# Performance work log

Hardware: AMD Instinct MI355X
Metric: run time of the kernel (lower is better)

## Reference

```python
import jax, jax.numpy as jnp
import numpy as np

B, D, N, H = 4, 512, 1536, 8
DIM = D // H  # per-head dim = 64


def _conv1x1(x, w, b):
    # Conv1d(kernel_size=1): x [B, C, N], w [O, C], b [O]
    return jnp.einsum('oc,bcn->bon', w, x) + b[None, :, None]


def setup_inputs() -> dict:
    key = jax.random.key(0)
    ks = jax.random.split(key, 13)
    s = 0.02
    return {
        'query': jax.random.normal(ks[0], (B, D, N), jnp.float32),
        'key': jax.random.normal(ks[1], (B, D, N), jnp.float32),
        'value': jax.random.normal(ks[2], (B, D, N), jnp.float32),
        'dist': jax.random.uniform(ks[3], (B, N, N), jnp.float32),
        'mask': jax.random.bernoulli(ks[4], 0.9, (N, N)),  # bool [N, M]
        'Wq': jax.random.normal(ks[5], (D, D), jnp.float32) * s,
        'bq': jnp.zeros((D,), jnp.float32),
        'Wk': jax.random.normal(ks[6], (D, D), jnp.float32) * s,
        'bk': jnp.zeros((D,), jnp.float32),
        'Wv': jax.random.normal(ks[7], (D, D), jnp.float32) * s,
        'bv': jnp.zeros((D,), jnp.float32),
        'Wm': jax.random.normal(ks[8], (D, D), jnp.float32) * s,
        'bm': jnp.zeros((D,), jnp.float32),
    }


def reference(query, key, value, dist, mask, Wq, bq, Wk, bk, Wv, bv, Wm, bm):
    # dist is accepted but unused, exactly as in the original forward.
    q = _conv1x1(query, Wq, bq).reshape(B, DIM, H, N)
    k = _conv1x1(key, Wk, bk).reshape(B, DIM, H, N)
    v = _conv1x1(value, Wv, bv).reshape(B, DIM, H, N)
    scores = jnp.einsum('bdhn,bdhm->bhnm', q, k) / jnp.sqrt(jnp.float32(DIM))
    # custom additive mask: (detached global min - 20) on masked-out positions
    pen = (jax.lax.stop_gradient(scores.min()) - 20.0) * (~mask).astype(scores.dtype)
    scores = scores + pen[None, None]  # broadcast over [B, H]
    prob = jax.nn.softmax(scores, axis=-1)
    x = jnp.einsum('bhnm,bdhm->bdhn', prob, v).reshape(B, D, N)
    out = _conv1x1(x, Wm, bm)
    return out, scores.mean(axis=1)
```

## Files before the change

### kernel.cpp

```cpp
#include <hip/hip_runtime.h>
#include <hip/hip_bf16.h>

typedef __hip_bfloat16 bf16;
typedef __attribute__((ext_vector_type(8))) short s16x8;
typedef __attribute__((ext_vector_type(4))) float f32x4;
typedef unsigned char uchar;

#define B_   4
#define D_   512
#define N_   1536
#define H_   8
#define DIM_ 64
#define NN_  (N_*N_)
#define BIGNEG (-30000.0f)

#define MFMA(a,b,c) __builtin_amdgcn_mfma_f32_16x16x32_bf16((a),(b),(c),0,0,0)

__device__ __forceinline__ short b16(float x){ bf16 h = __float2bfloat16(x); return *reinterpret_cast<short*>(&h); }

__device__ __forceinline__ s16x8 w8(const float* p){
  float4 u = *(const float4*)p, v = *(const float4*)(p+4);
  s16x8 r;
  r[0]=b16(u.x); r[1]=b16(u.y); r[2]=b16(u.z); r[3]=b16(u.w);
  r[4]=b16(v.x); r[5]=b16(v.y); r[6]=b16(v.z); r[7]=b16(v.w);
  return r;
}

__device__ unsigned detect_w4(const uchar* __restrict__ mraw, int* sh, int t){
  if (t == 0){ sh[0] = 0; sh[1] = 0; }
  __syncthreads();
  int a = 0, bb = 0;
  for (int i = t; i < 4096; i += 256){
    uchar v = mraw[i];
    if (v > 1) a = 1;
    else if (v && (i & 3)) bb = 1;
  }
  if (a)  atomicOr(&sh[0], 1);
  if (bb) atomicOr(&sh[1], 1);
  __syncthreads();
  return sh[0] ? 1u : (sh[1] ? 0u : 1u);
}

__global__ void detect_k(const uchar* __restrict__ mraw, unsigned* __restrict__ flags){
  __shared__ int sh[2];
  unsigned w4 = detect_w4(mraw, sh, threadIdx.x);
  if (threadIdx.x == 0) flags[0] = w4;
}

__global__ __launch_bounds__(256) void cvtW_k(const float* __restrict__ W0, const float* __restrict__ W1,
                                              const float* __restrict__ W2, const float* __restrict__ W3,
                                              bf16* __restrict__ dst){
  const float* src = (blockIdx.y==0)?W0:(blockIdx.y==1)?W1:(blockIdx.y==2)?W2:W3;
  bf16* d = dst + (size_t)blockIdx.y*(D_*D_);
  int i = (blockIdx.x*256 + threadIdx.x)*4;
  float4 v = *(const float4*)(src + i);
  __align__(8) short tmp[4] = {b16(v.x), b16(v.y), b16(v.z), b16(v.w)};
  *(int2*)((short*)d + i) = *(const int2*)tmp;
}

__device__ __forceinline__ void load_mt(uchar (*mt)[64], const void* mraw, unsigned w4,
                                        int n0, int m0, int t){
  int row = t >> 2, c = (t & 3) * 16;
  if (!w4){
    *(int4*)&mt[row][c] = *(const int4*)((const uchar*)mraw + (size_t)(n0 + row)*N_ + m0 + c);
  } else {
    const unsigned* mp = (const unsigned*)mraw + (size_t)(n0 + row)*N_ + m0 + c;
    uchar tmp[16];
    #pragma unroll
    for (int j = 0; j < 16; ++j) tmp[j] = mp[j] ? 1 : 0;
    *(int4*)&mt[row][c] = *(const int4*)tmp;
  }
}

__device__ __forceinline__ int mask_at(const void* mraw, unsigned w4, int n, int m){
  if (w4) return ((const unsigned*)mraw)[(size_t)n*N_ + m] != 0;
  return ((const uchar*)mraw)[(size_t)n*N_ + m] != 0;
}

template<int WBF>
__global__ __launch_bounds__(256) void convQKf_k(const float* __restrict__ X, const float* __restrict__ Wf,
                                                 const bf16* __restrict__ Wb,
                                                 const float* __restrict__ bias, bf16* __restrict__ dst,
                                                 float scale){
  int b = blockIdx.z, ot = blockIdx.y, nt = blockIdx.x;
  int t = threadIdx.x, w = t >> 6, L = t & 63, g = L >> 4, q = L & 15;
  __shared__ short Xs[64][72];
  __shared__ short tile[64][72];
  f32x4 acc[4] = {};
  float4 pf[4];
  #pragma unroll
  for (int it = 0; it < 4; ++it){
    int i = it*256 + t, cc = i >> 4, nq = (i & 15)*4;
    pf[it] = *(const float4*)(X + ((size_t)b*D_ + cc)*N_ + nt*64 + nq);
  }
  for (int cs = 0; cs < 8; ++cs){
    __syncthreads();
    #pragma unroll
    for (int it = 0; it < 4; ++it){
      int i = it*256 + t, cc = i >> 4, nq = (i & 15)*4;
      Xs[nq+0][cc] = b16(pf[it].x); Xs[nq+1][cc] = b16(pf[it].y);
      Xs[nq+2][cc] = b16(pf[it].z); Xs[nq+3][cc] = b16(pf[it].w);
    }
    if (cs < 7){
      #pragma unroll
      for (int it = 0; it < 4; ++it){
        int i = it*256 + t, cc = i >> 4, nq = (i & 15)*4;
        pf[it] = *(const float4*)(X + ((size_t)b*D_ + (cs+1)*64 + cc)*N_ + nt*64 + nq);
      }
    }
    __syncthreads();
    #pragma unroll
    for (int kk = 0; kk < 64; kk += 32){
      s16x8 a = *(const s16x8*)&Xs[w*16 + q][kk + 8*g];
      #pragma unroll
      for (int f = 0; f < 4; ++f){
        s16x8 bb;
        if (WBF) bb = *(const s16x8*)(Wb + (size_t)(ot*64 + f*16 + q)*D_ + cs*64 + kk + 8*g);
        else     bb = w8(Wf + (size_t)(ot*64 + f*16 + q)*D_ + cs*64 + kk + 8*g);
        acc[f] = MFMA(a, bb, acc[f]);
      }
    }
  }
  #pragma unroll
  for (int f = 0; f < 4; ++f){
    float bv = bias[ot*64 + f*16 + q];
    #pragma unroll
    for (int r = 0; r < 4; ++r)
      tile[w*16 + 4*g + r][f*16 + q] = b16((acc[f][r] + bv)*scale);
  }
  __syncthreads();
  #pragma unroll
  for (int it = 0; it < 2; ++it){
    int s = t + 256*it, row = s >> 3, h = s & 7;
    short tmp[8];
    #pragma unroll
    for (int j = 0; j < 8; ++j) tmp[j] = tile[row][h + 8*j];
    *(int4*)((short*)dst + ((size_t)(b*8+h)*N_ + nt*64 + row)*DIM_ + ot*8) = *(const int4*)tmp;
  }
}

template<int WBF>
__global__ __launch_bounds__(256) void convVf_k(const float* __restrict__ X, const float* __restrict__ Wf,
                                                const bf16* __restrict__ Wb,
                                                const float* __restrict__ bias, bf16* __restrict__ dst){
  int b = blockIdx.z, ot = blockIdx.y, nt = blockIdx.x;
  int t = threadIdx.x, w = t >> 6, L = t & 63, g = L >> 4, q = L & 15;
  __shared__ short Xs[64][72];
  __shared__ short tile[64][72];
  f32x4 acc[4] = {};
  float4 pf[4];
  #pragma unroll
  for (int it = 0; it < 4; ++it){
    int i = it*256 + t, cc = i >> 4, nq = (i & 15)*4;
    pf[it] = *(const float4*)(X + ((size_t)b*D_ + cc)*N_ + nt*64 + nq);
  }
  for (int cs = 0; cs < 8; ++cs){
    __syncthreads();
    #pragma unroll
    for (int it = 0; it < 4; ++it){
      int i = it*256 + t, cc = i >> 4, nq = (i & 15)*4;
      Xs[nq+0][cc] = b16(pf[it].x); Xs[nq+1][cc] = b16(pf[it].y);
      Xs[nq+2][cc] = b16(pf[it].z); Xs[nq+3][cc] = b16(pf[it].w);
    }
    if (cs < 7){
      #pragma unroll
      for (int it = 0; it < 4; ++it){
        int i = it*256 + t, cc = i >> 4, nq = (i & 15)*4;
        pf[it] = *(const float4*)(X + ((size_t)b*D_ + (cs+1)*64 + cc)*N_ + nt*64 + nq);
      }
    }
    __syncthreads();
    #pragma unroll
    for (int kk = 0; kk < 64; kk += 32){
      s16x8 a = *(const s16x8*)&Xs[w*16 + q][kk + 8*g];
      #pragma unroll
      for (int f = 0; f < 4; ++f){
        s16x8 bb;
        if (WBF) bb = *(const s16x8*)(Wb + (size_t)(ot*64 + f*16 + q)*D_ + cs*64 + kk + 8*g);
        else     bb = w8(Wf + (size_t)(ot*64 + f*16 + q)*D_ + cs*64 + kk + 8*g);
        acc[f] = MFMA(a, bb, acc[f]);
      }
    }
  }
  #pragma unroll
  for (int f = 0; f < 4; ++f){
    float bv = bias[ot*64 + f*16 + q];
    #pragma unroll
    for (int r = 0; r < 4; ++r)
      tile[w*16 + 4*g + r][f*16 + q] = b16(acc[f][r] + bv);
  }
  __syncthreads();
  int col = t & 63, seg = t >> 6;
  int h = col & 7, d = ot*8 + (col >> 3);
  short tmp[16];
  #pragma unroll
  for (int j = 0; j < 16; ++j) tmp[j] = tile[seg*16 + j][col];
  short* p = (short*)dst + ((size_t)(b*8+h)*DIM_ + d)*N_ + nt*64 + seg*16;
  *(int4*)p       = *(const int4*)&tmp[0];
  *(int4*)(p + 8) = *(const int4*)&tmp[8];
}

__global__ __launch_bounds__(256) void passA_k(const bf16* __restrict__ QH, const bf16* __restrict__ KH,
                                               float* __restrict__ out2f, float* __restrict__ bmin){
  int b = blockIdx.z, ntb = blockIdx.y, mtb = blockIdx.x;
  int t = threadIdx.x, w = t >> 6, L = t & 63, g = L >> 4, q = L & 15;
  __shared__ short Ks[2][64][72];
  int r0 = t >> 3, s0 = (t & 7)*8, r1 = (t + 256) >> 3;
  f32x4 mean[4] = {};
  float vmin = 3.4e38f;
  {
    const bf16* kb = KH + ((size_t)(b*H_)*N_ + mtb*64)*DIM_;
    *(int4*)&Ks[0][r0][s0] = *(const int4*)(kb + (size_t)r0*DIM_ + s0);
    *(int4*)&Ks[0][r1][s0] = *(const int4*)(kb + (size_t)r1*DIM_ + s0);
  }
  const bf16* qrow0 = QH + ((size_t)(b*H_)*N_ + ntb*64 + w*16 + q)*DIM_;
  s16x8 qa0 = *(const s16x8*)(qrow0 + 8*g);
  s16x8 qa1 = *(const s16x8*)(qrow0 + 32 + 8*g);
  int4 kn0, kn1; s16x8 qn0, qn1;
  {
    const bf16* kb = KH + ((size_t)(b*H_ + 1)*N_ + mtb*64)*DIM_;
    kn0 = *(const int4*)(kb + (size_t)r0*DIM_ + s0);
    kn1 = *(const int4*)(kb + (size_t)r1*DIM_ + s0);
    const bf16* qrow = QH + ((size_t)(b*H_ + 1)*N_ + ntb*64 + w*16 + q)*DIM_;
    qn0 = *(const s16x8*)(qrow + 8*g);
    qn1 = *(const s16x8*)(qrow + 32 + 8*g);
  }
  __syncthreads();
  for (int h = 0; h < H_; ++h){
    f32x4 acc[4] = {};
    #pragma unroll
    for (int f = 0; f < 4; ++f){
      acc[f] = MFMA(qa0, *(const s16x8*)&Ks[h&1][f*16 + q][8*g], acc[f]);
      acc[f] = MFMA(qa1, *(const s16x8*)&Ks[h&1][f*16 + q][32 + 8*g], acc[f]);
    }
    if (h < H_-1){
      *(int4*)&Ks[(h+1)&1][r0][s0] = kn0;
      *(int4*)&Ks[(h+1)&1][r1][s0] = kn1;
      qa0 = qn0; qa1 = qn1;
      if (h < H_-2){
        const bf16* kb = KH + ((size_t)(b*H_ + h+2)*N_ + mtb*64)*DIM_;
        kn0 = *(const int4*)(kb + (size_t)r0*DIM_ + s0);
        kn1 = *(const int4*)(kb + (size_t)r1*DIM_ + s0);
        const bf16* qrow = QH + ((size_t)(b*H_ + h+2)*N_ + ntb*64 + w*16 + q)*DIM_;
        qn0 = *(const s16x8*)(qrow + 8*g);
        qn1 = *(const s16x8*)(qrow + 32 + 8*g);
      }
    }
    #pragma unroll
    for (int f = 0; f < 4; ++f){
      #pragma unroll
      for (int r = 0; r < 4; ++r) vmin = fminf(vmin, acc[f][r]);
      mean[f] += acc[f];
    }
    __syncthreads();
  }
  #pragma unroll
  for (int off = 32; off; off >>= 1) vmin = fminf(vmin, __shfl_xor(vmin, off));
  __shared__ float wmin[4];
  if (L == 0) wmin[w] = vmin;
  __syncthreads();
  if (t == 0)
    bmin[((size_t)b*24 + ntb)*24 + mtb] = fminf(fminf(wmin[0],wmin[1]), fminf(wmin[2],wmin[3]));
  #pragma unroll
  for (int f = 0; f < 4; ++f)
    #pragma unroll
    for (int r = 0; r < 4; ++r)
      out2f[(size_t)b*NN_ + (size_t)(ntb*64 + w*16 + 4*g + r)*N_ + mtb*64 + f*16 + q]
        = mean[f][r] * 0.125f;
}

__global__ void minred_k(const float* __restrict__ bmin, float* __restrict__ penp){
  int t = threadIdx.x;
  float m = 3.4e38f;
  for (int i = t; i < 2304; i += 256) m = fminf(m, bmin[i]);
  #pragma unroll
  for (int off = 32; off; off >>= 1) m = fminf(m, __shfl_xor(m, off));
  __shared__ float wm[4];
  if ((t & 63) == 0) wm[t >> 6] = m;
  __syncthreads();
  if (t == 0) penp[0] = fminf(fminf(wm[0],wm[1]), fminf(wm[2],wm[3])) - 20.0f;
}

__global__ __launch_bounds__(256) void passCf_k(const void* __restrict__ mraw,
                                                const unsigned* __restrict__ flags,
                                                const float* __restrict__ penp,
                                                float* __restrict__ out2f){
  int i = blockIdx.x*256 + threadIdx.x;
  if (i >= NN_) return;
  int keep = flags[0] ? (((const unsigned*)mraw)[i] != 0) : (((const uchar*)mraw)[i] != 0);
  if (keep) return;
  float pen = penp[0];
  #pragma unroll
  for (int b = 0; b < B_; ++b) out2f[(size_t)b*NN_ + i] += pen;
}

__global__ __launch_bounds__(256) void passB_k(const bf16* __restrict__ QH, const bf16* __restrict__ KH,
                                               const bf16* __restrict__ VT, const void* __restrict__ mraw,
                                               bf16* __restrict__ xT){
  int b = blockIdx.z, h = blockIdx.y, ntb = blockIdx.x;
  int t = threadIdx.x, w = t >> 6, L = t & 63, g = L >> 4, q = L & 15;
  __shared__ short Ks[64][72], Vs[64][72];
  __shared__ uchar mt[64][64];
  __shared__ short P[4][16][72];
  __shared__ int dsh[2];
  unsigned w4 = detect_w4((const uchar*)mraw, dsh, t);
  size_t bh = (size_t)(b*H_ + h);
  const bf16* kbase = KH + bh*N_*DIM_;
  const bf16* vbase = VT + bh*(size_t)DIM_*N_;
  const bf16* qrow = QH + (bh*N_ + ntb*64 + w*16 + q)*DIM_;
  s16x8 qa0 = *(const s16x8*)(qrow + 8*g);
  s16x8 qa1 = *(const s16x8*)(qrow + 32 + 8*g);
  int r0 = t >> 3, s0 = (t & 7)*8, r1 = (t + 256) >> 3;
  int mrow = t >> 2, mc = (t & 3)*16;
  int4 kreg0, kreg1, vreg0, vreg1, mreg4[4];
  float lacc[4] = {0.f,0.f,0.f,0.f};
  f32x4 O[4] = {};
  {
    kreg0 = *(const int4*)(kbase + (size_t)r0*DIM_ + s0);
    kreg1 = *(const int4*)(kbase + (size_t)r1*DIM_ + s0);
    vreg0 = *(const int4*)(vbase + (size_t)r0*N_ + s0);
    vreg1 = *(const int4*)(vbase + (size_t)r1*N_ + s0);
    if (!w4) mreg4[0] = *(const int4*)((const uchar*)mraw + (size_t)(ntb*64 + mrow)*N_ + mc);
    else {
      const int4* mp = (const int4*)((const unsigned*)mraw + (size_t)(ntb*64 + mrow)*N_ + mc);
      #pragma unroll
      for (int j = 0; j < 4; ++j) mreg4[j] = mp[j];
    }
  }
  for (int mtb = 0; mtb < 24; ++mtb){
    __syncthreads();
    *(int4*)&Ks[r0][s0] = kreg0;
    *(int4*)&Ks[r1][s0] = kreg1;
    *(int4*)&Vs[r0][s0] = vreg0;
    *(int4*)&Vs[r1][s0] = vreg1;
    if (!w4) *(int4*)&mt[mrow][mc] = mreg4[0];
    else {
      uchar tmp[16];
      #pragma unroll
      for (int j = 0; j < 16; ++j) tmp[j] = ((const unsigned*)mreg4)[j] ? 1 : 0;
      *(int4*)&mt[mrow][mc] = *(const int4*)tmp;
    }
    if (mtb < 23){
      int m0 = (mtb+1)*64;
      kreg0 = *(const int4*)(kbase + (size_t)(m0 + r0)*DIM_ + s0);
      kreg1 = *(const int4*)(kbase + (size_t)(m0 + r1)*DIM_ + s0);
      vreg0 = *(const int4*)(vbase + (size_t)r0*N_ + m0 + s0);
      vreg1 = *(const int4*)(vbase + (size_t)r1*N_ + m0 + s0);
      if (!w4) mreg4[0] = *(const int4*)((const uchar*)mraw + (size_t)(ntb*64 + mrow)*N_ + m0 + mc);
      else {
        const int4* mp = (const int4*)((const unsigned*)mraw + (size_t)(ntb*64 + mrow)*N_ + m0 + mc);
        #pragma unroll
        for (int j = 0; j < 4; ++j) mreg4[j] = mp[j];
      }
    }
    __syncthreads();
    f32x4 acc[4] = {};
    #pragma unroll
    for (int f = 0; f < 4; ++f){
      acc[f] = MFMA(qa0, *(const s16x8*)&Ks[f*16 + q][8*g], acc[f]);
      acc[f] = MFMA(qa1, *(const s16x8*)&Ks[f*16 + q][32 + 8*g], acc[f]);
    }
    float pv[4][4];
    #pragma unroll
    for (int f = 0; f < 4; ++f)
      #pragma unroll
      for (int r = 0; r < 4; ++r)
        pv[f][r] = mt[w*16 + 4*g + r][f*16 + q] ? __expf(acc[f][r]) : 0.0f;
    #pragma unroll
    for (int r = 0; r < 4; ++r)
      lacc[r] += (pv[0][r] + pv[1][r]) + (pv[2][r] + pv[3][r]);
    #pragma unroll
    for (int f = 0; f < 4; ++f)
      #pragma unroll
      for (int r = 0; r < 4; ++r)
        P[w][4*g + r][f*16 + q] = b16(pv[f][r]);
    #pragma unroll
    for (int f2 = 0; f2 < 4; ++f2){
      O[f2] = MFMA(*(const s16x8*)&P[w][q][8*g],      *(const s16x8*)&Vs[f2*16 + q][8*g],      O[f2]);
      O[f2] = MFMA(*(const s16x8*)&P[w][q][32 + 8*g], *(const s16x8*)&Vs[f2*16 + q][32 + 8*g], O[f2]);
    }
  }
  #pragma unroll
  for (int r = 0; r < 4; ++r){
    #pragma unroll
    for (int off = 1; off < 16; off <<= 1) lacc[r] += __shfl_xor(lacc[r], off);
  }
  float inv[4];
  #pragma unroll
  for (int r = 0; r < 4; ++r) inv[r] = 1.0f / lacc[r];
  #pragma unroll
  for (int f2 = 0; f2 < 4; ++f2)
    #pragma unroll
    for (int r = 0; r < 4; ++r){
      int n = ntb*64 + w*16 + 4*g + r, d = f2*16 + q;
      ((short*)xT)[((size_t)b*N_ + n)*D_ + d*8 + h] = b16(O[f2][r]*inv[r]);
    }
}

template<int WBF>
__global__ __launch_bounds__(256) void gemm2_k(const float* __restrict__ Wmf, const bf16* __restrict__ Wmb,
                                               const float* __restrict__ bm,
                                               const bf16* __restrict__ xT, float* __restrict__ out0f){
  int b = blockIdx.z, ot = blockIdx.y, nt = blockIdx.x;
  int t = threadIdx.x, w = t >> 6, L = t & 63, g = L >> 4, q = L & 15;
  f32x4 acc[4] = {};
  for (int kk = 0; kk < D_; kk += 32){
    s16x8 a;
    if (WBF) a = *(const s16x8*)(Wmb + (size_t)(ot*64 + w*16 + q)*D_ + kk + 8*g);
    else     a = w8(Wmf + (size_t)(ot*64 + w*16 + q)*D_ + kk + 8*g);
    #pragma unroll
    for (int f = 0; f < 4; ++f){
      s16x8 bb = *(const s16x8*)(xT + ((size_t)b*N_ + nt*64 + f*16 + q)*D_ + kk + 8*g);
      acc[f] = MFMA(a, bb, acc[f]);
    }
  }
  #pragma unroll
  for (int f = 0; f < 4; ++f)
    #pragma unroll
    for (int r = 0; r < 4; ++r){
      int o = ot*64 + w*16 + 4*g + r;
      out0f[((size_t)b*D_ + o)*N_ + nt*64 + f*16 + q] = acc[f][r] + bm[o];
    }
}

__global__ __launch_bounds__(256) void t64_k(const float* __restrict__ X, bf16* __restrict__ XT){
  int b = blockIdx.z, ct = blockIdx.y, nt = blockIdx.x, t = threadIdx.x;
  __shared__ bf16 T[64][72];
  #pragma unroll
  for (int it = 0; it < 4; ++it){
    int idx = t + 256*it, cc = idx >> 4, s = idx & 15;
    float4 v = *(const float4*)(X + ((size_t)b*D_ + ct*64 + cc)*N_ + nt*64 + s*4);
    T[cc][s*4+0] = __float2bfloat16(v.x);
    T[cc][s*4+1] = __float2bfloat16(v.y);
    T[cc][s*4+2] = __float2bfloat16(v.z);
    T[cc][s*4+3] = __float2bfloat16(v.w);
  }
  __syncthreads();
  #pragma unroll
  for (int it = 0; it < 2; ++it){
    int idx = t + 256*it, nn = idx >> 3, s = idx & 7;
    short tmp[8];
    #pragma unroll
    for (int j = 0; j < 8; ++j) tmp[j] = *(short*)&T[s*8 + j][nn];
    *(int4*)((short*)XT + ((size_t)b*N_ + nt*64 + nn)*D_ + ct*64 + s*8) = *(const int4*)tmp;
  }
}

__global__ __launch_bounds__(256) void convQK_k(const bf16* __restrict__ XT, const float* __restrict__ W,
                                                const float* __restrict__ bias, bf16* __restrict__ dst,
                                                float scale){
  int b = blockIdx.z, ot = blockIdx.y, nt = blockIdx.x;
  int t = threadIdx.x, w = t >> 6, L = t & 63, g = L >> 4, q = L & 15;
  const bf16* Arow = XT + ((size_t)b*N_ + nt*64 + w*16 + q)*D_;
  f32x4 acc[4] = {};
  for (int kk = 0; kk < D_; kk += 32){
    s16x8 a = *(const s16x8*)(Arow + kk + 8*g);
    #pragma unroll
    for (int f = 0; f < 4; ++f){
      s16x8 bb = w8(W + (size_t)(ot*64 + f*16 + q)*D_ + kk + 8*g);
      acc[f] = MFMA(a, bb, acc[f]);
    }
  }
  __shared__ short tile[64][72];
  #pragma unroll
  for (int f = 0; f < 4; ++f){
    float bv = bias[ot*64 + f*16 + q];
    #pragma unroll
    for (int r = 0; r < 4; ++r)
      tile[w*16 + 4*g + r][f*16 + q] = b16((acc[f][r] + bv)*scale);
  }
  __syncthreads();
  #pragma unroll
  for (int it = 0; it < 2; ++it){
    int s = t + 256*it, row = s >> 3, h = s & 7;
    short tmp[8];
    #pragma unroll
    for (int j = 0; j < 8; ++j) tmp[j] = tile[row][h + 8*j];
    *(int4*)((short*)dst + ((size_t)(b*8+h)*N_ + nt*64 + row)*DIM_ + ot*8) = *(const int4*)tmp;
  }
}

__global__ __launch_bounds__(256) void convV_k(const bf16* __restrict__ XT, const float* __restrict__ W,
                                               const float* __restrict__ bias, bf16* __restrict__ dst){
  int b = blockIdx.z, ot = blockIdx.y, nt = blockIdx.x;
  int t = threadIdx.x, w = t >> 6, L = t & 63, g = L >> 4, q = L & 15;
  const bf16* Arow = XT + ((size_t)b*N_ + nt*64 + w*16 + q)*D_;
  f32x4 acc[4] = {};
  for (int kk = 0; kk < D_; kk += 32){
    s16x8 a = *(const s16x8*)(Arow + kk + 8*g);
    #pragma unroll
    for (int f = 0; f < 4; ++f){
      s16x8 bb = w8(W + (size_t)(ot*64 + f*16 + q)*D_ + kk + 8*g);
      acc[f] = MFMA(a, bb, acc[f]);
    }
  }
  __shared__ short tile[64][72];
  #pragma unroll
  for (int f = 0; f < 4; ++f){
    float bv = bias[ot*64 + f*16 + q];
    #pragma unroll
    for (int r = 0; r < 4; ++r)
      tile[w*16 + 4*g + r][f*16 + q] = b16(acc[f][r] + bv);
  }
  __syncthreads();
  int col = t & 63, seg = t >> 6;
  int h = col & 7, d = ot*8 + (col >> 3);
  short tmp[16];
  #pragma unroll
  for (int j = 0; j < 16; ++j) tmp[j] = tile[seg*16 + j][col];
  short* p = (short*)dst + ((size_t)(b*8+h)*DIM_ + d)*N_ + nt*64 + seg*16;
  *(int4*)p       = *(const int4*)&tmp[0];
  *(int4*)(p + 8) = *(const int4*)&tmp[8];
}

__global__ __launch_bounds__(256) void min_k(const bf16* __restrict__ QH, const bf16* __restrict__ KH,
                                             float* __restrict__ bmin){
  int b = blockIdx.z, ntb = blockIdx.y, mtb = blockIdx.x;
  int t = threadIdx.x, w = t >> 6, L = t & 63, g = L >> 4, q = L & 15;
  float vmin = 3.4e38f;
  for (int h = 0; h < H_; ++h){
    size_t bh = (size_t)(b*H_ + h);
    const bf16* qrow = QH + (bh*N_ + ntb*64 + w*16 + q)*DIM_;
    const bf16* krow = KH + (bh*N_ + mtb*64 + q)*DIM_;
    f32x4 acc[4] = {};
    #pragma unroll
    for (int kk = 0; kk < 64; kk += 32){
      s16x8 a = *(const s16x8*)(qrow + kk + 8*g);
      #pragma unroll
      for (int f = 0; f < 4; ++f){
        s16x8 bb = *(const s16x8*)(krow + (size_t)f*16*DIM_ + kk + 8*g);
        acc[f] = MFMA(a, bb, acc[f]);
      }
    }
    #pragma unroll
    for (int f = 0; f < 4; ++f)
      #pragma unroll
      for (int r = 0; r < 4; ++r) vmin = fminf(vmin, acc[f][r]);
  }
  #pragma unroll
  for (int off = 32; off; off >>= 1) vmin = fminf(vmin, __shfl_xor(vmin, off));
  __shared__ float wmin[4];
  if (L == 0) wmin[w] = vmin;
  __syncthreads();
  if (t == 0)
    bmin[((size_t)b*24 + ntb)*24 + mtb] = fminf(fminf(wmin[0],wmin[1]), fminf(wmin[2],wmin[3]));
}

__global__ __launch_bounds__(256) void meanLow_k(const bf16* __restrict__ QH, const bf16* __restrict__ KH,
                                                 const void* __restrict__ mraw, const float* __restrict__ penp,
                                                 float* __restrict__ out2f){
  int mtb = blockIdx.x, rt = blockIdx.y;
  if (rt == 48 && mtb == 0) return;
  __shared__ uchar mt[64][64];
  __shared__ int dsh[2];
  int t = threadIdx.x, w = t >> 6, L = t & 63, g = L >> 4, q = L & 15;
  unsigned w4 = detect_w4((const uchar*)mraw, dsh, t);
  int gr = rt*64, b = gr / N_, n0 = gr % N_;
  load_mt(mt, mraw, w4, n0, mtb*64, t);
  __syncthreads();
  float pen = penp[0];
  f32x4 mean[4] = {};
  for (int h = 0; h < H_; ++h){
    size_t bh = (size_t)(b*H_ + h);
    const bf16* qrow = QH + (bh*N_ + n0 + w*16 + q)*DIM_;
    const bf16* krow = KH + (bh*N_ + mtb*64 + q)*DIM_;
    f32x4 acc[4] = {};
    #pragma unroll
    for (int kk = 0; kk < 64; kk += 32){
      s16x8 a = *(const s16x8*)(qrow + kk + 8*g);
      #pragma unroll
      for (int f = 0; f < 4; ++f){
        s16x8 bb = *(const s16x8*)(krow + (size_t)f*16*DIM_ + kk + 8*g);
        acc[f] = MFMA(a, bb, acc[f]);
      }
    }
    #pragma unroll
    for (int f = 0; f < 4; ++f) mean[f] += acc[f];
  }
  #pragma unroll
  for (int f = 0; f < 4; ++f)
    #pragma unroll
    for (int r = 0; r < 4; ++r){
      float v = mean[f][r]*0.125f;
      if (!mt[w*16 + 4*g + r][f*16 + q]) v += pen;
      out2f[(size_t)b*NN_ + (size_t)(n0 + w*16 + 4*g + r)*N_ + mtb*64 + f*16 + q] = v;
    }
}

__device__ void build_head(const float* __restrict__ X, const float* __restrict__ W,
                           const float* __restrict__ bias, int b, int n0, int h,
                           short (*dst)[72], short (*Xs)[72], int t){
  int w = t >> 6, L = t & 63, g = L >> 4, q = L & 15;
  f32x4 acc[4] = {};
  for (int cs = 0; cs < 8; ++cs){
    __syncthreads();
    #pragma unroll
    for (int it = 0; it < 4; ++it){
      int i = it*256 + t, cc = i >> 4, nq = (i & 15)*4;
      float4 v = *(const float4*)(X + ((size_t)b*D_ + cs*64 + cc)*N_ + n0 + nq);
      Xs[nq+0][cc] = b16(v.x); Xs[nq+1][cc] = b16(v.y);
      Xs[nq+2][cc] = b16(v.z); Xs[nq+3][cc] = b16(v.w);
    }
    __syncthreads();
    #pragma unroll
    for (int kk = 0; kk < 64; kk += 32){
      s16x8 a = w8(W + (size_t)((w*16 + q)*8 + h)*D_ + cs*64 + kk + 8*g);
      #pragma unroll
      for (int f = 0; f < 4; ++f){
        s16x8 bb = *(const s16x8*)&Xs[f*16 + q][kk + 8*g];
        acc[f] = MFMA(a, bb, acc[f]);
      }
    }
  }
  __syncthreads();
  #pragma unroll
  for (int f = 0; f < 4; ++f)
    #pragma unroll
    for (int r = 0; r < 4; ++r){
      int d = w*16 + 4*g + r, n = f*16 + q;
      dst[n][d] = b16(acc[f][r] + bias[d*8 + h]);
    }
  __syncthreads();
}

__global__ __launch_bounds__(256) void meanHigh_k(const float* __restrict__ Xq, const float* __restrict__ Wq,
                                                  const float* __restrict__ bq,
                                                  const float* __restrict__ Xk, const float* __restrict__ Wk,
                                                  const float* __restrict__ bk,
                                                  const void* __restrict__ mraw, const float* __restrict__ penp,
                                                  float* __restrict__ out2f){
  __shared__ short qt[64][72], kt[64][72], Xs[64][72];
  __shared__ int dsh[2];
  int t = threadIdx.x, w = t >> 6, L = t & 63, g = L >> 4, q = L & 15;
  unsigned w4 = detect_w4((const uchar*)mraw, dsh, t);
  int rt = 64 + blockIdx.y, gr = rt*64, b = gr / N_, n0 = gr % N_;
  float pen = penp[0];
  f32x4 mean[6][4] = {};
  for (int h = 0; h < H_; ++h){
    build_head(Xq, Wq, bq, b, n0, h, qt, Xs, t);
    for (int mi = 0; mi < 6; ++mi){
      int m0 = (blockIdx.x*6 + mi)*64;
      build_head(Xk, Wk, bk, b, m0, h, kt, Xs, t);
      f32x4 acc[4] = {};
      #pragma unroll
      for (int kk = 0; kk < 64; kk += 32){
        s16x8 a = *(const s16x8*)&qt[w*16 + q][kk + 8*g];
        #pragma unroll
        for (int f = 0; f < 4; ++f){
          s16x8 bb = *(const s16x8*)&kt[f*16 + q][kk + 8*g];
          acc[f] = MFMA(a, bb, acc[f]);
        }
      }
      #pragma unroll
      for (int f = 0; f < 4; ++f) mean[mi][f] += acc[f]*0.125f;
    }
  }
  for (int mi = 0; mi < 6; ++mi){
    int m0 = (blockIdx.x*6 + mi)*64;
    #pragma unroll
    for (int f = 0; f < 4; ++f)
      #pragma unroll
      for (int r = 0; r < 4; ++r){
        int n = n0 + w*16 + 4*g + r, m = m0 + f*16 + q;
        float v = mean[mi][f][r]*0.125f;
        if (!mask_at(mraw, w4, n, m)) v += pen;
        out2f[(size_t)b*NN_ + (size_t)n*N_ + m] = v;
      }
  }
}

__global__ __launch_bounds__(256) void meanFinal_k(const float* __restrict__ Xq, const float* __restrict__ Wq,
                                                   const float* __restrict__ bq,
                                                   const float* __restrict__ Xk, const float* __restrict__ Wk,
                                                   const float* __restrict__ bk,
                                                   const void* __restrict__ mraw, const float* __restrict__ penp,
                                                   float* __restrict__ out2f){
  __shared__ short qt[64][72], kt[64][72], Xs[64][72];
  __shared__ int dsh[2];
  int t = threadIdx.x, w = t >> 6, L = t & 63, g = L >> 4, q = L & 15;
  unsigned w4 = detect_w4((const uchar*)mraw, dsh, t);
  float pen = penp[0];
  const int b = 2, n0 = 0, m0 = 0;
  f32x4 mean[4] = {};
  for (int h = 0; h < H_; ++h){
    build_head(Xq, Wq, bq, b, n0, h, qt, Xs, t);
    build_head(Xk, Wk, bk, b, m0, h, kt, Xs, t);
    f32x4 acc[4] = {};
    #pragma unroll
    for (int kk = 0; kk < 64; kk += 32){
      s16x8 a = *(const s16x8*)&qt[w*16 + q][kk + 8*g];
      #pragma unroll
      for (int f = 0; f < 4; ++f){
        s16x8 bb = *(const s16x8*)&kt[f*16 + q][kk + 8*g];
        acc[f] = MFMA(a, bb, acc[f]);
      }
    }
    #pragma unroll
    for (int f = 0; f < 4; ++f) mean[f] += acc[f]*0.125f;
  }
  #pragma unroll
  for (int f = 0; f < 4; ++f)
    #pragma unroll
    for (int r = 0; r < 4; ++r){
      int n = n0 + w*16 + 4*g + r, m = m0 + f*16 + q;
      float v = mean[f][r]*0.125f;
      if (!mask_at(mraw, w4, n, m)) v += pen;
      out2f[(size_t)b*NN_ + (size_t)n*N_ + m] = v;
    }
}

extern "C" void kernel_launch(void* const* d_in, const int* in_sizes, int n_in,
                              void* d_out, int out_size, void* d_ws, size_t ws_size,
                              hipStream_t stream) {
  (void)in_sizes; (void)n_in; (void)out_size;
  const float* query = (const float*)d_in[0];
  const float* key   = (const float*)d_in[1];
  const float* value = (const float*)d_in[2];
  const void*  mraw  = d_in[4];
  const float* Wq = (const float*)d_in[5],  *bq = (const float*)d_in[6];
  const float* Wk = (const float*)d_in[7],  *bk = (const float*)d_in[8];
  const float* Wv = (const float*)d_in[9],  *bv = (const float*)d_in[10];
  const float* Wm = (const float*)d_in[11], *bm = (const float*)d_in[12];

  const size_t E = (size_t)B_*D_*N_;
  float* out0f = (float*)d_out;
  float* out2f = out0f + E;
  char*  base  = (char*)d_out;

  const size_t WB     = (size_t)4*D_*D_*sizeof(bf16);
  const size_t needF  = 16384 + 4*E;
  const size_t needF2 = 16384 + WB + 4*E;

  if (ws_size >= needF){
    const bool wbf = (ws_size >= needF2);
    char* ws = (char*)d_ws;
    unsigned* flags = (unsigned*)ws;
    float* penp = (float*)(ws + 64);
    float* bmin = (float*)(ws + 256);
    bf16* Wb  = (bf16*)(ws + 16384);
    bf16* S_Q = wbf ? (bf16*)(ws + 16384 + WB) : (bf16*)(ws + 16384);
    bf16* S_K = S_Q + E;
    bf16* S_V = (bf16*)(base + 8*E);
    bf16* S_X = (bf16*)(base + 10*E);

    detect_k<<<1, 256, 0, stream>>>((const uchar*)mraw, flags);

    if (wbf){
      cvtW_k<<<dim3(D_*D_/1024, 4), 256, 0, stream>>>(Wq, Wk, Wv, Wm, Wb);
      convQKf_k<1><<<dim3(24,8,B_), 256, 0, stream>>>(query, Wq, Wb,            bq, S_Q, 0.125f);
      convQKf_k<1><<<dim3(24,8,B_), 256, 0, stream>>>(key,   Wk, Wb + (size_t)D_*D_,   bk, S_K, 1.0f);
      convVf_k <1><<<dim3(24,8,B_), 256, 0, stream>>>(value, Wv, Wb + (size_t)2*D_*D_, bv, S_V);
    } else {
      convQKf_k<0><<<dim3(24,8,B_), 256, 0, stream>>>(query, Wq, nullptr, bq, S_Q, 0.125f);
      convQKf_k<0><<<dim3(24,8,B_), 256, 0, stream>>>(key,   Wk, nullptr, bk, S_K, 1.0f);
      convVf_k <0><<<dim3(24,8,B_), 256, 0, stream>>>(value, Wv, nullptr, bv, S_V);
    }

    passB_k <<<dim3(24,8,B_), 256, 0, stream>>>(S_Q, S_K, S_V, mraw, S_X);
    if (wbf) gemm2_k<1><<<dim3(24,8,B_), 256, 0, stream>>>(Wm, Wb + (size_t)3*D_*D_, bm, S_X, out0f);
    else     gemm2_k<0><<<dim3(24,8,B_), 256, 0, stream>>>(Wm, nullptr,              bm, S_X, out0f);

    passA_k <<<dim3(24,24,B_), 256, 0, stream>>>(S_Q, S_K, out2f, bmin);
    minred_k<<<1, 256, 0, stream>>>(bmin, penp);
    passCf_k<<<NN_/256, 256, 0, stream>>>(mraw, flags, penp, out2f);
  } else {
    bf16* S_V = (bf16*)(base + 8*E);
    bf16* S_X = (bf16*)(base + 10*E);
    bf16* S_Q = (bf16*)(base + 12*E);
    bf16* S_K = (bf16*)(base + 14*E);
    float* penp = (float*)S_X;
    float* bmin = (float*)(base + 10*E + 256);

    t64_k   <<<dim3(24,8,B_), 256, 0, stream>>>(query, S_X);
    convQK_k<<<dim3(24,8,B_), 256, 0, stream>>>(S_X, Wq, bq, S_Q, 0.125f);
    t64_k   <<<dim3(24,8,B_), 256, 0, stream>>>(key, S_X);
    convQK_k<<<dim3(24,8,B_), 256, 0, stream>>>(S_X, Wk, bk, S_K, 1.0f);
    t64_k   <<<dim3(24,8,B_), 256, 0, stream>>>(value, S_X);
    convV_k <<<dim3(24,8,B_), 256, 0, stream>>>(S_X, Wv, bv, S_V);

    passB_k <<<dim3(24,8,B_), 256, 0, stream>>>(S_Q, S_K, S_V, mraw, S_X);
    gemm2_k<0><<<dim3(24,8,B_), 256, 0, stream>>>(Wm, nullptr, bm, S_X, out0f);

    min_k   <<<dim3(24,24,B_), 256, 0, stream>>>(S_Q, S_K, bmin);
    minred_k<<<1, 256, 0, stream>>>(bmin, penp);

    meanLow_k  <<<dim3(24,64), 256, 0, stream>>>(S_Q, S_K, mraw, penp, out2f);
    meanHigh_k <<<dim3(4,32),  256, 0, stream>>>(query, Wq, bq, key, Wk, bk, mraw, penp, out2f);
    meanFinal_k<<<1, 256, 0, stream>>>(query, Wq, bq, key, Wk, bk, mraw, penp, out2f);
  }
}
```

Measured before the change: 250.1 us.

## Split attention over key halves with merge pass and fuse QKV projections

Merges the three Q/K/V projection launches into one kernel with a 12-deep z grid, so a single launch has more blocks in flight. Attention is split across two halves of the key dimension (flash-decoding style). Each half writes unnormalized bf16 partial outputs and row sums, and a new merge kernel adds and normalizes them into the transposed layout. The goal is to double the attention grid to fill the GPU better and to drop the per-block mask detection. The cost is an extra merge pass with bf16 rounding of the partials. The split softmax also skips max subtraction and relies on small score magnitudes.

```diff
diff --git a/kernel.cpp b/kernel.cpp
--- a/kernel.cpp
+++ b/kernel.cpp
@@ -12,11 +12,11 @@
 #define H_   8
 #define DIM_ 64
 #define NN_  (N_*N_)
-#define BIGNEG (-30000.0f)
 
 #define MFMA(a,b,c) __builtin_amdgcn_mfma_f32_16x16x32_bf16((a),(b),(c),0,0,0)
 
 __device__ __forceinline__ short b16(float x){ bf16 h = __float2bfloat16(x); return *reinterpret_cast<short*>(&h); }
+__device__ __forceinline__ float f16f(short s){ bf16 h = *reinterpret_cast<bf16*>(&s); return __bfloat162float(h); }
 
 __device__ __forceinline__ s16x8 w8(const float* p){
   float4 u = *(const float4*)p, v = *(const float4*)(p+4);
@@ -77,13 +77,18 @@
   return ((const uchar*)mraw)[(size_t)n*N_ + m] != 0;
 }
 
-template<int WBF>
-__global__ __launch_bounds__(256) void convQKf_k(const float* __restrict__ X, const float* __restrict__ Wf,
-                                                 const bf16* __restrict__ Wb,
-                                                 const float* __restrict__ bias, bf16* __restrict__ dst,
-                                                 float scale){
-  int b = blockIdx.z, ot = blockIdx.y, nt = blockIdx.x;
-  int t = threadIdx.x, w = t >> 6, L = t & 63, g = L >> 4, q = L & 15;
+__global__ __launch_bounds__(256) void convAll_k(const float* __restrict__ Xq, const float* __restrict__ Xk,
+                                                 const float* __restrict__ Xv, const bf16* __restrict__ Wb,
+                                                 const float* __restrict__ bq, const float* __restrict__ bk,
+                                                 const float* __restrict__ bv,
+                                                 bf16* __restrict__ SQ, bf16* __restrict__ SK, bf16* __restrict__ SV){
+  int z = blockIdx.z, which = z >> 2, b = z & 3;
+  int ot = blockIdx.y, nt = blockIdx.x;
+  int t = threadIdx.x, w = t >> 6, L = t & 63, g = L >> 4, q = L & 15;
+  const float* X    = which==0 ? Xq : which==1 ? Xk : Xv;
+  const bf16*  W    = Wb + (size_t)which*D_*D_;
+  const float* bias = which==0 ? bq : which==1 ? bk : bv;
+  float scale = which==0 ? 0.125f : 1.0f;
   __shared__ short Xs[64][72];
   __shared__ short tile[64][72];
   f32x4 acc[4] = {};
@@ -114,35 +119,44 @@
       s16x8 a = *(const s16x8*)&Xs[w*16 + q][kk + 8*g];
       #pragma unroll
       for (int f = 0; f < 4; ++f){
-        s16x8 bb;
-        if (WBF) bb = *(const s16x8*)(Wb + (size_t)(ot*64 + f*16 + q)*D_ + cs*64 + kk + 8*g);
-        else     bb = w8(Wf + (size_t)(ot*64 + f*16 + q)*D_ + cs*64 + kk + 8*g);
+        s16x8 bb = *(const s16x8*)(W + (size_t)(ot*64 + f*16 + q)*D_ + cs*64 + kk + 8*g);
         acc[f] = MFMA(a, bb, acc[f]);
       }
     }
   }
   #pragma unroll
   for (int f = 0; f < 4; ++f){
-    float bv = bias[ot*64 + f*16 + q];
+    float bv2 = bias[ot*64 + f*16 + q];
     #pragma unroll
     for (int r = 0; r < 4; ++r)
-      tile[w*16 + 4*g + r][f*16 + q] = b16((acc[f][r] + bv)*scale);
-  }
-  __syncthreads();
-  #pragma unroll
-  for (int it = 0; it < 2; ++it){
-    int s = t + 256*it, row = s >> 3, h = s & 7;
-    short tmp[8];
-    #pragma unroll
-    for (int j = 0; j < 8; ++j) tmp[j] = tile[row][h + 8*j];
-    *(int4*)((short*)dst + ((size_t)(b*8+h)*N_ + nt*64 + row)*DIM_ + ot*8) = *(const int4*)tmp;
-  }
-}
-
-template<int WBF>
-__global__ __launch_bounds__(256) void convVf_k(const float* __restrict__ X, const float* __restrict__ Wf,
-                                                const bf16* __restrict__ Wb,
-                                                const float* __restrict__ bias, bf16* __restrict__ dst){
+      tile[w*16 + 4*g + r][f*16 + q] = b16((acc[f][r] + bv2)*scale);
+  }
+  __syncthreads();
+  if (which < 2){
+    bf16* dst = which==0 ? SQ : SK;
+    #pragma unroll
+    for (int it = 0; it < 2; ++it){
+      int s = t + 256*it, row = s >> 3, h = s & 7;
+      short tmp[8];
+      #pragma unroll
+      for (int j = 0; j < 8; ++j) tmp[j] = tile[row][h + 8*j];
+      *(int4*)((short*)dst + ((size_t)(b*8+h)*N_ + nt*64 + row)*DIM_ + ot*8) = *(const int4*)tmp;
+    }
+  } else {
+    int col = t & 63, seg = t >> 6;
+    int h = col & 7, d = ot*8 + (col >> 3);
+    short tmp[16];
+    #pragma unroll
+    for (int j = 0; j < 16; ++j) tmp[j] = tile[seg*16 + j][col];
+    short* p = (short*)SV + ((size_t)(b*8+h)*DIM_ + d)*N_ + nt*64 + seg*16;
+    *(int4*)p       = *(const int4*)&tmp[0];
+    *(int4*)(p + 8) = *(const int4*)&tmp[8];
+  }
+}
+
+__global__ __launch_bounds__(256) void convQKf_k(const float* __restrict__ X, const float* __restrict__ Wf,
+                                                 const float* __restrict__ bias, bf16* __restrict__ dst,
+                                                 float scale){
   int b = blockIdx.z, ot = blockIdx.y, nt = blockIdx.x;
   int t = threadIdx.x, w = t >> 6, L = t & 63, g = L >> 4, q = L & 15;
   __shared__ short Xs[64][72];
@@ -175,9 +189,64 @@
       s16x8 a = *(const s16x8*)&Xs[w*16 + q][kk + 8*g];
       #pragma unroll
       for (int f = 0; f < 4; ++f){
-        s16x8 bb;
-        if (WBF) bb = *(const s16x8*)(Wb + (size_t)(ot*64 + f*16 + q)*D_ + cs*64 + kk + 8*g);
-        else     bb = w8(Wf + (size_t)(ot*64 + f*16 + q)*D_ + cs*64 + kk + 8*g);
+        s16x8 bb = w8(Wf + (size_t)(ot*64 + f*16 + q)*D_ + cs*64 + kk + 8*g);
+        acc[f] = MFMA(a, bb, acc[f]);
+      }
+    }
+  }
+  #pragma unroll
+  for (int f = 0; f < 4; ++f){
+    float bv = bias[ot*64 + f*16 + q];
+    #pragma unroll
+    for (int r = 0; r < 4; ++r)
+      tile[w*16 + 4*g + r][f*16 + q] = b16((acc[f][r] + bv)*scale);
+  }
+  __syncthreads();
+  #pragma unroll
+  for (int it = 0; it < 2; ++it){
+    int s = t + 256*it, row = s >> 3, h = s & 7;
+    short tmp[8];
+    #pragma unroll
+    for (int j = 0; j < 8; ++j) tmp[j] = tile[row][h + 8*j];
+    *(int4*)((short*)dst + ((size_t)(b*8+h)*N_ + nt*64 + row)*DIM_ + ot*8) = *(const int4*)tmp;
+  }
+}
+
+__global__ __launch_bounds__(256) void convVf_k(const float* __restrict__ X, const float* __restrict__ Wf,
+                                                const float* __restrict__ bias, bf16* __restrict__ dst){
+  int b = blockIdx.z, ot = blockIdx.y, nt = blockIdx.x;
+  int t = threadIdx.x, w = t >> 6, L = t & 63, g = L >> 4, q = L & 15;
+  __shared__ short Xs[64][72];
+  __shared__ short tile[64][72];
+  f32x4 acc[4] = {};
+  float4 pf[4];
+  #pragma unroll
+  for (int it = 0; it < 4; ++it){
+    int i = it*256 + t, cc = i >> 4, nq = (i & 15)*4;
+    pf[it] = *(const float4*)(X + ((size_t)b*D_ + cc)*N_ + nt*64 + nq);
+  }
+  for (int cs = 0; cs < 8; ++cs){
+    __syncthreads();
+    #pragma unroll
+    for (int it = 0; it < 4; ++it){
+      int i = it*256 + t, cc = i >> 4, nq = (i & 15)*4;
+      Xs[nq+0][cc] = b16(pf[it].x); Xs[nq+1][cc] = b16(pf[it].y);
+      Xs[nq+2][cc] = b16(pf[it].z); Xs[nq+3][cc] = b16(pf[it].w);
+    }
+    if (cs < 7){
+      #pragma unroll
+      for (int it = 0; it < 4; ++it){
+        int i = it*256 + t, cc = i >> 4, nq = (i & 15)*4;
+        pf[it] = *(const float4*)(X + ((size_t)b*D_ + (cs+1)*64 + cc)*N_ + nt*64 + nq);
+      }
+    }
+    __syncthreads();
+    #pragma unroll
+    for (int kk = 0; kk < 64; kk += 32){
+      s16x8 a = *(const s16x8*)&Xs[w*16 + q][kk + 8*g];
+      #pragma unroll
+      for (int f = 0; f < 4; ++f){
+        s16x8 bb = w8(Wf + (size_t)(ot*64 + f*16 + q)*D_ + cs*64 + kk + 8*g);
         acc[f] = MFMA(a, bb, acc[f]);
       }
     }
@@ -292,6 +361,135 @@
   float pen = penp[0];
   #pragma unroll
   for (int b = 0; b < B_; ++b) out2f[(size_t)b*NN_ + i] += pen;
+}
+
+__global__ __launch_bounds__(256) void passBs_k(const bf16* __restrict__ QH, const bf16* __restrict__ KH,
+                                                const bf16* __restrict__ VT, const void* __restrict__ mraw,
+                                                const unsigned* __restrict__ flags,
+                                                bf16* __restrict__ Opart, float* __restrict__ lpart){
+  int z = blockIdx.z, half = z >> 2, b = z & 3;
+  int h = blockIdx.y, ntb = blockIdx.x;
+  int t = threadIdx.x, w = t >> 6, L = t & 63, g = L >> 4, q = L & 15;
+  __shared__ short Ks[64][72], Vs[64][72];
+  __shared__ uchar mt[64][64];
+  __shared__ short P[4][16][72];
+  unsigned w4 = flags[0];
+  size_t bh = (size_t)(b*H_ + h);
+  const bf16* kbase = KH + bh*N_*DIM_;
+  const bf16* vbase = VT + bh*(size_t)DIM_*N_;
+  const bf16* qrow = QH + (bh*N_ + ntb*64 + w*16 + q)*DIM_;
+  s16x8 qa0 = *(const s16x8*)(qrow + 8*g);
+  s16x8 qa1 = *(const s16x8*)(qrow + 32 + 8*g);
+  int r0 = t >> 3, s0 = (t & 7)*8, r1 = (t + 256) >> 3;
+  int mrow = t >> 2, mc = (t & 3)*16;
+  int4 kreg0, kreg1, vreg0, vreg1, mreg4[4];
+  float lacc[4] = {0.f,0.f,0.f,0.f};
+  f32x4 O[4] = {};
+  int mt0 = half*12;
+  {
+    int m0 = mt0*64;
+    kreg0 = *(const int4*)(kbase + (size_t)(m0 + r0)*DIM_ + s0);
+    kreg1 = *(const int4*)(kbase + (size_t)(m0 + r1)*DIM_ + s0);
+    vreg0 = *(const int4*)(vbase + (size_t)r0*N_ + m0 + s0);
+    vreg1 = *(const int4*)(vbase + (size_t)r1*N_ + m0 + s0);
+    if (!w4) mreg4[0] = *(const int4*)((const uchar*)mraw + (size_t)(ntb*64 + mrow)*N_ + m0 + mc);
+    else {
+      const int4* mp = (const int4*)((const unsigned*)mraw + (size_t)(ntb*64 + mrow)*N_ + m0 + mc);
+      #pragma unroll
+      for (int j = 0; j < 4; ++j) mreg4[j] = mp[j];
+    }
+  }
+  for (int i = 0; i < 12; ++i){
+    __syncthreads();
+    *(int4*)&Ks[r0][s0] = kreg0;
+    *(int4*)&Ks[r1][s0] = kreg1;
+    *(int4*)&Vs[r0][s0] = vreg0;
+    *(int4*)&Vs[r1][s0] = vreg1;
+    if (!w4) *(int4*)&mt[mrow][mc] = mreg4[0];
+    else {
+      uchar tmp[16];
+      #pragma unroll
+      for (int j = 0; j < 16; ++j) tmp[j] = ((const unsigned*)mreg4)[j] ? 1 : 0;
+      *(int4*)&mt[mrow][mc] = *(const int4*)tmp;
+    }
+    if (i < 11){
+      int m0 = (mt0 + i + 1)*64;
+      kreg0 = *(const int4*)(kbase + (size_t)(m0 + r0)*DIM_ + s0);
+      kreg1 = *(const int4*)(kbase + (size_t)(m0 + r1)*DIM_ + s0);
+      vreg0 = *(const int4*)(vbase + (size_t)r0*N_ + m0 + s0);
+      vreg1 = *(const int4*)(vbase + (size_t)r1*N_ + m0 + s0);
+      if (!w4) mreg4[0] = *(const int4*)((const uchar*)mraw + (size_t)(ntb*64 + mrow)*N_ + m0 + mc);
+      else {
+        const int4* mp = (const int4*)((const unsigned*)mraw + (size_t)(ntb*64 + mrow)*N_ + m0 + mc);
+        #pragma unroll
+        for (int j = 0; j < 4; ++j) mreg4[j] = mp[j];
+      }
+    }
+    __syncthreads();
+    f32x4 acc[4] = {};
+    #pragma unroll
+    for (int f = 0; f < 4; ++f){
+      acc[f] = MFMA(qa0, *(const s16x8*)&Ks[f*16 + q][8*g], acc[f]);
+      acc[f] = MFMA(qa1, *(const s16x8*)&Ks[f*16 + q][32 + 8*g], acc[f]);
+    }
+    float pv[4][4];
+    #pragma unroll
+    for (int f = 0; f < 4; ++f)
+      #pragma unroll
+      for (int r = 0; r < 4; ++r)
+        pv[f][r] = mt[w*16 + 4*g + r][f*16 + q] ? __expf(acc[f][r]) : 0.0f;
+    #pragma unroll
+    for (int r = 0; r < 4; ++r)
+      lacc[r] += (pv[0][r] + pv[1][r]) + (pv[2][r] + pv[3][r]);
+    #pragma unroll
+    for (int f = 0; f < 4; ++f)
+      #pragma unroll
+      for (int r = 0; r < 4; ++r)
+        P[w][4*g + r][f*16 + q] = b16(pv[f][r]);
+    #pragma unroll
+    for (int f2 = 0; f2 < 4; ++f2){
+      O[f2] = MFMA(*(const s16x8*)&P[w][q][8*g],      *(const s16x8*)&Vs[f2*16 + q][8*g],      O[f2]);
+      O[f2] = MFMA(*(const s16x8*)&P[w][q][32 + 8*g], *(const s16x8*)&Vs[f2*16 + q][32 + 8*g], O[f2]);
+    }
+  }
+  #pragma unroll
+  for (int r = 0; r < 4; ++r){
+    #pragma unroll
+    for (int off = 1; off < 16; off <<= 1) lacc[r] += __shfl_xor(lacc[r], off);
+  }
+  bf16* Op = Opart + (size_t)half*((size_t)B_*H_*N_*DIM_);
+  float* lp = lpart + (size_t)half*((size_t)B_*H_*N_);
+  if (q == 0){
+    #pragma unroll
+    for (int r = 0; r < 4; ++r)
+      lp[bh*N_ + ntb*64 + w*16 + 4*g + r] = lacc[r];
+  }
+  #pragma unroll
+  for (int f2 = 0; f2 < 4; ++f2)
+    #pragma unroll
+    for (int r = 0; r < 4; ++r){
+      int n = ntb*64 + w*16 + 4*g + r, d = f2*16 + q;
+      ((short*)Op)[(bh*N_ + n)*DIM_ + d] = b16(O[f2][r]);
+    }
+}
+
+__global__ __launch_bounds__(256) void merge_k(const bf16* __restrict__ Opart, const float* __restrict__ lpart,
+                                               bf16* __restrict__ xT){
+  int b = blockIdx.z, h = blockIdx.y, nt = blockIdx.x, t = threadIdx.x;
+  int nl = t >> 3, d0 = (t & 7)*8;
+  int n = nt*32 + nl;
+  size_t bh = (size_t)(b*H_ + h);
+  size_t row = bh*N_ + n;
+  const size_t OS = (size_t)B_*H_*N_*DIM_, LS = (size_t)B_*H_*N_;
+  float inv = 1.0f / (lpart[row] + lpart[LS + row]);
+  int4 a = *(const int4*)((const short*)Opart + row*DIM_ + d0);
+  int4 c = *(const int4*)((const short*)Opart + OS*1 + row*DIM_ + d0);
+  const short* as = (const short*)&a;
+  const short* cs = (const short*)&c;
+  short* out = (short*)xT + ((size_t)b*N_ + n)*D_ + h;
+  #pragma unroll
+  for (int j = 0; j < 8; ++j)
+    out[(size_t)(d0 + j)*8] = b16((f16f(as[j]) + f16f(cs[j])) * inv);
 }
 
 __global__ __launch_bounds__(256) void passB_k(const bf16* __restrict__ QH, const bf16* __restrict__ KH,
@@ -727,12 +925,15 @@
   float* out2f = out0f + E;
   char*  base  = (char*)d_out;
 
-  const size_t WB     = (size_t)4*D_*D_*sizeof(bf16);
-  const size_t needF  = 16384 + 4*E;
-  const size_t needF2 = 16384 + WB + 4*E;
+  const size_t WB      = (size_t)4*D_*D_*sizeof(bf16);
+  const size_t LPART   = (size_t)2*B_*H_*N_*sizeof(float);
+  const size_t needF   = 16384 + 4*E;
+  const size_t needF2  = 16384 + WB + 4*E;
+  const size_t needF3  = needF2 + LPART;
 
   if (ws_size >= needF){
-    const bool wbf = (ws_size >= needF2);
+    const bool wbf   = (ws_size >= needF2);
+    const bool split = (ws_size >= needF3);
     char* ws = (char*)d_ws;
     unsigned* flags = (unsigned*)ws;
     float* penp = (float*)(ws + 64);
@@ -740,23 +941,28 @@
     bf16* Wb  = (bf16*)(ws + 16384);
     bf16* S_Q = wbf ? (bf16*)(ws + 16384 + WB) : (bf16*)(ws + 16384);
     bf16* S_K = S_Q + E;
+    float* lpart = (float*)((char*)(S_K + E));
     bf16* S_V = (bf16*)(base + 8*E);
     bf16* S_X = (bf16*)(base + 10*E);
+    bf16* Opart = (bf16*)(base + 12*E);
 
     detect_k<<<1, 256, 0, stream>>>((const uchar*)mraw, flags);
 
     if (wbf){
       cvtW_k<<<dim3(D_*D_/1024, 4), 256, 0, stream>>>(Wq, Wk, Wv, Wm, Wb);
-      convQKf_k<1><<<dim3(24,8,B_), 256, 0, stream>>>(query, Wq, Wb,            bq, S_Q, 0.125f);
-      convQKf_k<1><<<dim3(24,8,B_), 256, 0, stream>>>(key,   Wk, Wb + (size_t)D_*D_,   bk, S_K, 1.0f);
-      convVf_k <1><<<dim3(24,8,B_), 256, 0, stream>>>(value, Wv, Wb + (size_t)2*D_*D_, bv, S_V);
+      convAll_k<<<dim3(24,8,12), 256, 0, stream>>>(query, key, value, Wb, bq, bk, bv, S_Q, S_K, S_V);
     } else {
-      convQKf_k<0><<<dim3(24,8,B_), 256, 0, stream>>>(query, Wq, nullptr, bq, S_Q, 0.125f);
-      convQKf_k<0><<<dim3(24,8,B_), 256, 0, stream>>>(key,   Wk, nullptr, bk, S_K, 1.0f);
-      convVf_k <0><<<dim3(24,8,B_), 256, 0, stream>>>(value, Wv, nullptr, bv, S_V);
-    }
-
-    passB_k <<<dim3(24,8,B_), 256, 0, stream>>>(S_Q, S_K, S_V, mraw, S_X);
+      convQKf_k<<<dim3(24,8,B_), 256, 0, stream>>>(query, Wq, bq, S_Q, 0.125f);
+      convQKf_k<<<dim3(24,8,B_), 256, 0, stream>>>(key,   Wk, bk, S_K, 1.0f);
+      convVf_k <<<dim3(24,8,B_), 256, 0, stream>>>(value, Wv, bv, S_V);
+    }
+
+    if (split){
+      passBs_k<<<dim3(24,8,8), 256, 0, stream>>>(S_Q, S_K, S_V, mraw, flags, Opart, lpart);
+      merge_k <<<dim3(48,8,B_), 256, 0, stream>>>(Opart, lpart, S_X);
+    } else {
+      passB_k <<<dim3(24,8,B_), 256, 0, stream>>>(S_Q, S_K, S_V, mraw, S_X);
+    }
     if (wbf) gemm2_k<1><<<dim3(24,8,B_), 256, 0, stream>>>(Wm, Wb + (size_t)3*D_*D_, bm, S_X, out0f);
     else     gemm2_k<0><<<dim3(24,8,B_), 256, 0, stream>>>(Wm, nullptr,              bm, S_X, out0f);
 
```

Result: slower. 258.1 us (+3.2%).
